# Optimization experiments

Measured on AMD Instinct MI355X. Metric: run time of the kernel, lower is better.

## Reference

```python
import jax, jax.numpy as jnp
import numpy as np

DT_SCALER = 1.0 / 24.0
ODE_STEPS = 4  # fixed-step RK4 stand-in for adaptive odeint(rtol=atol=1e-3)
B, T, D, H = 1024, 100, 32, 256
ODE_MID = 50  # hidden width of the ODE func MLP (hard-coded 50 in source)


def setup_inputs() -> dict:
    key = jax.random.key(0)
    ks = jax.random.split(key, 20)
    n = lambda k, s: jax.random.normal(k, s, dtype=jnp.float32)
    std = 0.1  # module inits weights N(0, 0.1), biases 0
    return {
        "dt": jax.random.uniform(ks[0], (B, T, 2), dtype=jnp.float32),
        "x": n(ks[1], (B, T, D)),
        # RNNCell params
        "W_ih": n(ks[2], (H, D)) * std,
        "b_ih": jnp.zeros((H,), jnp.float32),
        "W_hh": n(ks[3], (H, H)) * std,
        "b_hh": jnp.zeros((H,), jnp.float32),
        # ODE func: Linear(H,50) -> tanh -> Linear(50,H)
        "ode_w1": n(ks[4], (ODE_MID, H)) * std,
        "ode_b1": jnp.zeros((ODE_MID,), jnp.float32),
        "ode_w2": n(ks[5], (H, ODE_MID)) * std,
        "ode_b2": jnp.zeros((H,), jnp.float32),
        # mu head: l1 (H -> H//2), distribution_mu (H//2 -> 1)
        "l1_w": n(ks[6], (H // 2, H)) * std,
        "l1_b": jnp.zeros((H // 2,), jnp.float32),
        "mu_w": n(ks[7], (1, H // 2)) * std,
        "mu_b": jnp.zeros((1,), jnp.float32),
        # sigma head: Linear(H,H) -> tanh -> Linear(H,1) -> softplus
        "sig_w1": n(ks[8], (H, H)) * std,
        "sig_b1": jnp.zeros((H,), jnp.float32),
        "sig_w2": n(ks[9], (1, H)) * std,
        "sig_b2": jnp.zeros((1,), jnp.float32),
    }


def reference(dt, x, W_ih, b_ih, W_hh, b_hh, ode_w1, ode_b1, ode_w2, ode_b2,
              l1_w, l1_b, mu_w, mu_b, sig_w1, sig_b1, sig_w2, sig_b2):
    Bsz = x.shape[0]
    xs = jnp.swapaxes(x, 0, 1)                               # [T,B,D]
    dts = jnp.swapaxes(dt[:, :, 1] - dt[:, :, 0], 0, 1)[..., None]  # [T,B,1]
    h0 = jnp.zeros((Bsz, W_hh.shape[0]), x.dtype)
    hs = 1.0 / ODE_STEPS

    def ode_f(y, scale):
        # net(y) * (dt * DT_SCALER); RHS is time-independent
        return (jnp.tanh(y @ ode_w1.T + ode_b1) @ ode_w2.T + ode_b2) * scale

    def step(h, inp):
        x_i, dt_i = inp                                      # [B,D], [B,1]
        # h_t = h_t + RNNCell(x_i, h_t)
        h = h + jnp.tanh(x_i @ W_ih.T + b_ih + h @ W_hh.T + b_hh)
        scale = dt_i * DT_SCALER
        # integrate dh/dt = ode_f(h) from t=0 to t=1 (fixed-step RK4)
        def rk4(y, _):
            k1 = ode_f(y, scale)
            k2 = ode_f(y + 0.5 * hs * k1, scale)
            k3 = ode_f(y + 0.5 * hs * k2, scale)
            k4 = ode_f(y + hs * k3, scale)
            return y + (hs / 6.0) * (k1 + 2.0 * k2 + 2.0 * k3 + k4), None
        h, _ = jax.lax.scan(rk4, h, None, length=ODE_STEPS)
        # heads (eval mode: dropout is identity)
        mu = jax.nn.relu(h @ l1_w.T + l1_b) @ mu_w.T + mu_b              # [B,1]
        sig = jax.nn.softplus(jnp.tanh(h @ sig_w1.T + sig_b1) @ sig_w2.T + sig_b2)
        return h, (mu, sig)

    _, (mu_seq, sig_seq) = jax.lax.scan(step, h0, (xs, dts))
    mu_out = jnp.swapaxes(mu_seq, 0, 1)    # [B,T,1]
    sig_out = jnp.swapaxes(sig_seq, 0, 1)  # [B,T,1]
    return (mu_out, sig_out)
```

## Files before the change

### kernel.cpp

```cpp
#include <hip/hip_runtime.h>
#include <math.h>


#define NT 512

#define WF_WCAT 0
#define WF_L1   18432
#define WF_SG   26624

#define F4_YC   0
#define F4_MID  128
#define F4_HL   160
#define F4_X    416
#define F4_L1O  432
#define F4_SG   496
#define SM_L1B  2496
#define SM_SB1  2624
#define SM_MUW  2880
#define SM_SW2  3008
#define SM_SCL  3264
#define SM_TOTF 3272

__device__ __forceinline__ float fma4(float acc, float4 y, float4 w) {
  acc = fmaf(y.x, w.x, acc); acc = fmaf(y.y, w.y, acc);
  acc = fmaf(y.z, w.z, acc); acc = fmaf(y.w, w.w, acc);
  return acc;
}
__device__ __forceinline__ float4 add4(float4 a, float4 b) {
  return make_float4(a.x + b.x, a.y + b.y, a.z + b.z, a.w + b.w);
}
__device__ __forceinline__ float4 axpy4(float a, float4 xv, float4 yv) {
  return make_float4(fmaf(a, xv.x, yv.x), fmaf(a, xv.y, yv.y),
                     fmaf(a, xv.z, yv.z), fmaf(a, xv.w, yv.w));
}
__device__ __forceinline__ float4 muls4(float4 v, float s) {
  return make_float4(v.x * s, v.y * s, v.z * s, v.w * s);
}
__device__ __forceinline__ float tfast(float x) {
  float ax = fabsf(x);
  float e  = __expf(-2.f * ax);
  float t  = (1.f - e) * __builtin_amdgcn_rcpf(1.f + e);
  return copysignf(t, x);
}
__device__ __forceinline__ float4 tfast4(float4 v) {
  return make_float4(tfast(v.x), tfast(v.y), tfast(v.z), tfast(v.w));
}

template <int CTRL>
__device__ __forceinline__ float dpp_add(float v) {
  int s = __builtin_amdgcn_update_dpp(0, __float_as_int(v), CTRL, 0xF, 0xF, true);
  return v + __int_as_float(s);
}
__device__ __forceinline__ float red2(float v)  { return dpp_add<0xB1>(v); }
__device__ __forceinline__ float red4(float v)  { return dpp_add<0x4E>(dpp_add<0xB1>(v)); }
__device__ __forceinline__ float red8(float v)  {
  return dpp_add<0xB1>(dpp_add<0x4E>(dpp_add<0x141>(v)));
}
__device__ __forceinline__ float red16(float v) {
  return dpp_add<0xB1>(dpp_add<0x4E>(dpp_add<0x141>(dpp_add<0x140>(v))));
}

__global__ void prep_w(const float* __restrict__ Wih, const float* __restrict__ Whh,
                       const float* __restrict__ l1w, const float* __restrict__ sw1,
                       float* __restrict__ ws) {
  int i = blockIdx.x * 256 + threadIdx.x;
  if (i < 73728) {
    int fi = i >> 2, comp = i & 3;
    int j = fi >> 9, tw = fi & 511;
    int c = j / 9, gg = j - c * 9;
    int cq = tw >> 3, kc = tw & 7;
    int k = 36 * kc + 4 * gg + comp, col = 4 * cq + c;
    ws[i] = (k < 32) ? Wih[col * 32 + k] : Whh[col * 256 + (k - 32)];
  } else if (i < 73728 + 32768) {
    int t = i - 73728;
    int fi = t >> 2, comp = t & 3;
    int j = fi >> 7, tt = fi & 127;
    int c = j >> 4, jj = j & 15;
    int cq = tt >> 2, kc = tt & 3;
    int k = 4 * (4 * jj + kc) + comp, col = 4 * cq + c;
    ws[73728 + t] = l1w[col * 256 + k];
  } else if (i < 172032) {
    int t = i - 106496;
    int fi = t >> 2, comp = t & 3;
    int j = fi >> 7, tt = fi & 127;
    int c = j >> 5, jj = j & 31;
    int cq = tt >> 1, kc = tt & 1;
    int k = 4 * (2 * jj + kc) + comp, col = 4 * cq + c;
    ws[106496 + t] = sw1[col * 256 + k];
  }
}

__device__ __forceinline__ void rnn_phase(int tid, int pOld, const float4* __restrict__ wc4,
                                          float4* smf4, float4 bcR) {
  const int cq = tid >> 3, kc = tid & 7;
  float a0 = 0, a1 = 0, a2 = 0, a3 = 0, a4 = 0, a5 = 0, a6 = 0, a7 = 0;
#pragma unroll 1
  for (int gg = 0; gg < 9; ++gg) {
    int g = kc * 9 + gg;
    int i0 = (g < 8) ? (F4_X + g) : (F4_HL + pOld * 128 + (g - 8));
    int i1 = (g < 8) ? (F4_X + 8 + g) : (F4_HL + pOld * 128 + 64 + (g - 8));
    float4 y0 = smf4[i0];
    float4 y1 = smf4[i1];
    float4 w0 = wc4[(0 * 9 + gg) * 512 + tid];
    float4 w1 = wc4[(1 * 9 + gg) * 512 + tid];
    float4 w2 = wc4[(2 * 9 + gg) * 512 + tid];
    float4 w3 = wc4[(3 * 9 + gg) * 512 + tid];
    a0 = fma4(a0, y0, w0); a1 = fma4(a1, y0, w1);
    a2 = fma4(a2, y0, w2); a3 = fma4(a3, y0, w3);
    a4 = fma4(a4, y1, w0); a5 = fma4(a5, y1, w1);
    a6 = fma4(a6, y1, w2); a7 = fma4(a7, y1, w3);
  }
  a0 = red8(a0); a1 = red8(a1); a2 = red8(a2); a3 = red8(a3);
  a4 = red8(a4); a5 = red8(a5); a6 = red8(a6); a7 = red8(a7);
  if (kc == 0) {
    float4 h0 = smf4[F4_HL + pOld * 128 + cq];
    float4 h1 = smf4[F4_HL + pOld * 128 + 64 + cq];
    float4 n0 = add4(h0, tfast4(add4(make_float4(a0, a1, a2, a3), bcR)));
    float4 n1 = add4(h1, tfast4(add4(make_float4(a4, a5, a6, a7), bcR)));
    int pN = pOld ^ 1;
    smf4[F4_HL + pN * 128 + cq] = n0;
    smf4[F4_HL + pN * 128 + 64 + cq] = n1;
    smf4[F4_YC + cq] = n0;
    smf4[F4_YC + 64 + cq] = n1;
  }
}

__global__ __attribute__((amdgpu_flat_work_group_size(NT, NT)))
__attribute__((amdgpu_waves_per_eu(4)))
void odernn_main(const float* __restrict__ dt,
                 const float* __restrict__ x,
                 const float* __restrict__ bih,
                 const float* __restrict__ bhh,
                 const float* __restrict__ ow1,
                 const float* __restrict__ ob1g,
                 const float* __restrict__ ow2,
                 const float* __restrict__ ob2g,
                 const float* __restrict__ l1bg,
                 const float* __restrict__ muwg,
                 const float* __restrict__ mubg,
                 const float* __restrict__ sb1g,
                 const float* __restrict__ sw2g,
                 const float* __restrict__ sb2g,
                 const float* __restrict__ ws,
                 float* __restrict__ out) {
  __shared__ __align__(16) float sm[SM_TOTF];
  float4* smf4 = (float4*)sm;
  const int tid = threadIdx.x;
  const int b0 = blockIdx.x * 2;

  const float4* wc4  = (const float4*)ws + WF_WCAT;
  const float4* l1s4 = (const float4*)ws + WF_L1;
  const float4* sgs4 = (const float4*)ws + WF_SG;

  const int cqR = tid >> 3;
  float4 bcR = make_float4(bih[4 * cqR + 0] + bhh[4 * cqR + 0],
                           bih[4 * cqR + 1] + bhh[4 * cqR + 1],
                           bih[4 * cqR + 2] + bhh[4 * cqR + 2],
                           bih[4 * cqR + 3] + bhh[4 * cqR + 3]);

  if (tid < 128) { sm[SM_L1B + tid] = l1bg[tid]; sm[SM_MUW + tid] = muwg[tid]; }
  if (tid < 256) { sm[SM_SB1 + tid] = sb1g[tid]; sm[SM_SW2 + tid] = sw2g[tid]; }
  if (tid < 128) smf4[F4_HL + tid] = make_float4(0.f, 0.f, 0.f, 0.f);
  if (tid < 16) {
    int r = tid >> 3, g = tid & 7;
    smf4[F4_X + tid] = ((const float4*)x)[((size_t)(b0 + r) * 100) * 8 + g];
  } else if (tid < 18) {
    const float* dp = dt + ((size_t)(b0 + tid - 16) * 100) * 2;
    sm[SM_SCL + tid - 16] = (dp[1] - dp[0]) * (1.f / 24.f);
  }
  __syncthreads();

  if (tid < 256) {
    const int q1 = tid >> 4, kc1 = tid & 15;
    float4 w1r[16];
#pragma unroll
    for (int n = 0; n < 4; ++n) {
      int row = 4 * q1 + n;
#pragma unroll
      for (int j = 0; j < 4; ++j)
        w1r[n * 4 + j] = (row < 50)
            ? *(const float4*)&ow1[row * 256 + 64 * j + 4 * kc1]
            : make_float4(0.f, 0.f, 0.f, 0.f);
    }
    float4 ob1r = make_float4(4 * q1 + 0 < 50 ? ob1g[4 * q1 + 0] : 0.f,
                              4 * q1 + 1 < 50 ? ob1g[4 * q1 + 1] : 0.f,
                              4 * q1 + 2 < 50 ? ob1g[4 * q1 + 2] : 0.f,
                              4 * q1 + 3 < 50 ? ob1g[4 * q1 + 3] : 0.f);
    const int rH = tid >> 7, cqH = (tid >> 2) & 31, kcH = tid & 3;
    const int t7 = tid & 127;
    const float mubv = mubg[0];

    for (int t = 0; t < 100; ++t) {
      const int pOld = t & 1, pNew = pOld ^ 1;
      rnn_phase(tid, pOld, wc4, smf4, bcR);
      __syncthreads();
#pragma unroll 1
      for (int e = 0; e < 16; ++e) {
        float a0 = 0, a1 = 0, a2 = 0, a3 = 0, a4 = 0, a5 = 0, a6 = 0, a7 = 0;
#pragma unroll
        for (int j = 0; j < 4; ++j) {
          float4 y0 = smf4[F4_YC + 16 * j + kc1];
          float4 y1 = smf4[F4_YC + 64 + 16 * j + kc1];
          a0 = fma4(a0, y0, w1r[0 * 4 + j]); a1 = fma4(a1, y0, w1r[1 * 4 + j]);
          a2 = fma4(a2, y0, w1r[2 * 4 + j]); a3 = fma4(a3, y0, w1r[3 * 4 + j]);
          a4 = fma4(a4, y1, w1r[0 * 4 + j]); a5 = fma4(a5, y1, w1r[1 * 4 + j]);
          a6 = fma4(a6, y1, w1r[2 * 4 + j]); a7 = fma4(a7, y1, w1r[3 * 4 + j]);
        }
        a0 = red16(a0); a1 = red16(a1); a2 = red16(a2); a3 = red16(a3);
        a4 = red16(a4); a5 = red16(a5); a6 = red16(a6); a7 = red16(a7);
        if (kc1 == 0) {
          smf4[F4_MID + q1]      = tfast4(add4(make_float4(a0, a1, a2, a3), ob1r));
          smf4[F4_MID + 16 + q1] = tfast4(add4(make_float4(a4, a5, a6, a7), ob1r));
        }
        __syncthreads();
        __syncthreads();
      }
      float c0 = 0, c1 = 0, c2 = 0, c3 = 0;
#pragma unroll 2
      for (int jj = 0; jj < 16; ++jj) {
        float4 h = smf4[F4_HL + pNew * 128 + rH * 64 + 4 * jj + kcH];
        c0 = fma4(c0, h, l1s4[(0 * 16 + jj) * 128 + t7]);
        c1 = fma4(c1, h, l1s4[(1 * 16 + jj) * 128 + t7]);
        c2 = fma4(c2, h, l1s4[(2 * 16 + jj) * 128 + t7]);
        c3 = fma4(c3, h, l1s4[(3 * 16 + jj) * 128 + t7]);
      }
      c0 = red4(c0); c1 = red4(c1); c2 = red4(c2); c3 = red4(c3);
      if (kcH == 0) {
        float4 b = ((const float4*)(sm + SM_L1B))[cqH];
        float4 v = add4(make_float4(c0, c1, c2, c3), b);
        smf4[F4_L1O + rH * 32 + cqH] =
            make_float4(fmaxf(v.x, 0.f), fmaxf(v.y, 0.f), fmaxf(v.z, 0.f), fmaxf(v.w, 0.f));
      }
      if (t < 99) {
        if (tid < 16) {
          int r = tid >> 3, g = tid & 7;
          smf4[F4_X + tid] = ((const float4*)x)[((size_t)(b0 + r) * 100 + t + 1) * 8 + g];
        } else if (tid < 18) {
          const float* dp = dt + ((size_t)(b0 + tid - 16) * 100 + t + 1) * 2;
          sm[SM_SCL + tid - 16] = (dp[1] - dp[0]) * (1.f / 24.f);
        }
      }
      __syncthreads();
      int wv = tid >> 6, ln = tid & 63;
      if (wv < 2) {
        float pm = 0.f;
        if (ln < 32) {
          float4 l = smf4[F4_L1O + wv * 32 + ln];
          float4 w = ((const float4*)(sm + SM_MUW))[ln];
          pm = l.x * w.x + l.y * w.y + l.z * w.z + l.w * w.w;
        }
#pragma unroll
        for (int off = 32; off > 0; off >>= 1) pm += __shfl_down(pm, off);
        if (ln == 0) out[(size_t)(b0 + wv) * 100 + t] = pm + mubv;
      }
    }
  } else {
    const int tid2 = tid - 256;
    const int cqB = tid2 >> 2, kc2 = tid2 & 3;
    float4 w2r[16];
#pragma unroll
    for (int c = 0; c < 4; ++c) {
      int col = 4 * cqB + c;
#pragma unroll
      for (int j = 0; j < 4; ++j) {
        float w0v[4];
#pragma unroll
        for (int cc = 0; cc < 4; ++cc) {
          int k = 16 * j + 4 * kc2 + cc;
          w0v[cc] = (k < 50) ? ow2[col * 50 + k] : 0.f;
        }
        w2r[c * 4 + j] = make_float4(w0v[0], w0v[1], w0v[2], w0v[3]);
      }
    }
    float4 ob2r = make_float4(ob2g[4 * cqB + 0], ob2g[4 * cqB + 1],
                              ob2g[4 * cqB + 2], ob2g[4 * cqB + 3]);
    const int rH = tid2 >> 7, cqH = (tid2 >> 1) & 63, kcH = tid2 & 1;
    const int t7 = tid2 & 127;
    const float sb2v = sb2g[0];

    for (int t = 0; t < 100; ++t) {
      const int pOld = t & 1, pNew = pOld ^ 1;
      rnn_phase(tid, pOld, wc4, smf4, bcR);
      __syncthreads();
      float s0 = sm[SM_SCL + 0], s1 = sm[SM_SCL + 1];
      float4 h0 = smf4[F4_YC + cqB];
      float4 h1 = smf4[F4_YC + 64 + cqB];
      float4 ac0 = make_float4(0, 0, 0, 0), ac1 = ac0;
#pragma unroll 1
      for (int os = 0; os < 4; ++os) {
#pragma unroll
        for (int s = 0; s < 4; ++s) {
          __syncthreads();
          float b0 = 0, b1 = 0, b2 = 0, b3 = 0, b4 = 0, b5 = 0, b6 = 0, b7 = 0;
#pragma unroll
          for (int j = 0; j < 4; ++j) {
            float4 m0 = smf4[F4_MID + 4 * j + kc2];
            float4 m1 = smf4[F4_MID + 16 + 4 * j + kc2];
            b0 = fma4(b0, m0, w2r[0 * 4 + j]); b1 = fma4(b1, m0, w2r[1 * 4 + j]);
            b2 = fma4(b2, m0, w2r[2 * 4 + j]); b3 = fma4(b3, m0, w2r[3 * 4 + j]);
            b4 = fma4(b4, m1, w2r[0 * 4 + j]); b5 = fma4(b5, m1, w2r[1 * 4 + j]);
            b6 = fma4(b6, m1, w2r[2 * 4 + j]); b7 = fma4(b7, m1, w2r[3 * 4 + j]);
          }
          b0 = red4(b0); b1 = red4(b1); b2 = red4(b2); b3 = red4(b3);
          b4 = red4(b4); b5 = red4(b5); b6 = red4(b6); b7 = red4(b7);
          float4 k0 = muls4(add4(make_float4(b0, b1, b2, b3), ob2r), s0);
          float4 k1 = muls4(add4(make_float4(b4, b5, b6, b7), ob2r), s1);
          float4 y0w, y1w;
          if (s == 0) {
            ac0 = k0; ac1 = k1;
            y0w = axpy4(0.125f, k0, h0); y1w = axpy4(0.125f, k1, h1);
          } else if (s == 1) {
            ac0 = axpy4(2.f, k0, ac0); ac1 = axpy4(2.f, k1, ac1);
            y0w = axpy4(0.125f, k0, h0); y1w = axpy4(0.125f, k1, h1);
          } else if (s == 2) {
            ac0 = axpy4(2.f, k0, ac0); ac1 = axpy4(2.f, k1, ac1);
            y0w = axpy4(0.25f, k0, h0); y1w = axpy4(0.25f, k1, h1);
          } else {
            h0 = axpy4(0.25f / 6.f, add4(ac0, k0), h0);
            h1 = axpy4(0.25f / 6.f, add4(ac1, k1), h1);
            y0w = h0; y1w = h1;
          }
          if (kc2 == 0) {
            smf4[F4_YC + cqB] = y0w;
            smf4[F4_YC + 64 + cqB] = y1w;
            if (os == 3 && s == 3) {
              smf4[F4_HL + pNew * 128 + cqB] = h0;
              smf4[F4_HL + pNew * 128 + 64 + cqB] = h1;
            }
          }
          __syncthreads();
        }
      }
      float d0 = 0, d1 = 0, d2 = 0, d3 = 0;
#pragma unroll 2
      for (int jj = 0; jj < 32; ++jj) {
        float4 h = smf4[F4_HL + pNew * 128 + rH * 64 + 2 * jj + kcH];
        d0 = fma4(d0, h, sgs4[(0 * 32 + jj) * 128 + t7]);
        d1 = fma4(d1, h, sgs4[(1 * 32 + jj) * 128 + t7]);
        d2 = fma4(d2, h, sgs4[(2 * 32 + jj) * 128 + t7]);
        d3 = fma4(d3, h, sgs4[(3 * 32 + jj) * 128 + t7]);
      }
      d0 = red2(d0); d1 = red2(d1); d2 = red2(d2); d3 = red2(d3);
      if (kcH == 0) {
        float4 sb = ((const float4*)(sm + SM_SB1))[cqH];
        smf4[F4_SG + rH * 64 + cqH] = tfast4(add4(make_float4(d0, d1, d2, d3), sb));
      }
      __syncthreads();
      int wv = tid >> 6, ln = tid & 63;
      if (wv < 6) {
        int r = wv - 4;
        float4 sv = smf4[F4_SG + r * 64 + ln];
        float4 w = ((const float4*)(sm + SM_SW2))[ln];
        float ps = sv.x * w.x + sv.y * w.y + sv.z * w.z + sv.w * w.w;
#pragma unroll
        for (int off = 32; off > 0; off >>= 1) ps += __shfl_down(ps, off);
        if (ln == 0) {
          float z = ps + sb2v;
          float sp = fmaxf(z, 0.f) + log1pf(expf(-fabsf(z)));
          out[(size_t)102400 + (size_t)(b0 + r) * 100 + t] = sp;
        }
      }
    }
  }
}

extern "C" void kernel_launch(void* const* d_in, const int* in_sizes, int n_in,
                              void* d_out, int out_size, void* d_ws, size_t ws_size,
                              hipStream_t stream) {
  const float* dt  = (const float*)d_in[0];
  const float* x   = (const float*)d_in[1];
  const float* Wih = (const float*)d_in[2];
  const float* bih = (const float*)d_in[3];
  const float* Whh = (const float*)d_in[4];
  const float* bhh = (const float*)d_in[5];
  const float* ow1 = (const float*)d_in[6];
  const float* ob1 = (const float*)d_in[7];
  const float* ow2 = (const float*)d_in[8];
  const float* ob2 = (const float*)d_in[9];
  const float* l1w = (const float*)d_in[10];
  const float* l1b = (const float*)d_in[11];
  const float* muw = (const float*)d_in[12];
  const float* mub = (const float*)d_in[13];
  const float* sw1 = (const float*)d_in[14];
  const float* sb1 = (const float*)d_in[15];
  const float* sw2 = (const float*)d_in[16];
  const float* sb2 = (const float*)d_in[17];
  float* ws  = (float*)d_ws;
  float* out = (float*)d_out;

  prep_w<<<672, 256, 0, stream>>>(Wih, Whh, l1w, sw1, ws);
  odernn_main<<<512, NT, 0, stream>>>(dt, x, bih, bhh, ow1, ob1, ow2, ob2,
                                      l1b, muw, mub, sb1, sw2, sb2, ws, out);
}
```

Before: 3.806 ms.

## Process four batch rows per block with ping-pong ODE layer pipelining

New measurement: 4.371 ms. 1.15x slower.

```diff
diff --git a/kernel.cpp b/kernel.cpp
--- a/kernel.cpp
+++ b/kernel.cpp
@@ -8,18 +8,20 @@
 #define WF_L1   18432
 #define WF_SG   26624
 
-#define F4_YC   0
-#define F4_MID  128
-#define F4_HL   160
-#define F4_X    416
-#define F4_L1O  432
-#define F4_SG   496
-#define SM_L1B  2496
-#define SM_SB1  2624
-#define SM_MUW  2880
-#define SM_SW2  3008
-#define SM_SCL  3264
-#define SM_TOTF 3272
+#define F4_YCP  0
+#define F4_YCQ  128
+#define F4_MIDP 256
+#define F4_MIDQ 288
+#define F4_HL   320
+#define F4_X    832
+#define F4_L1O  896
+#define F4_SG   1024
+#define SM_L1B  5120
+#define SM_SB1  5248
+#define SM_MUW  5504
+#define SM_SW2  5632
+#define SM_SCL  5888
+#define SM_TOTF 5896
 
 __device__ __forceinline__ float fma4(float acc, float4 y, float4 w) {
   acc = fmaf(y.x, w.x, acc); acc = fmaf(y.y, w.y, acc);
@@ -45,7 +47,6 @@
 __device__ __forceinline__ float4 tfast4(float4 v) {
   return make_float4(tfast(v.x), tfast(v.y), tfast(v.z), tfast(v.w));
 }
-
 template <int CTRL>
 __device__ __forceinline__ float dpp_add(float v) {
   int s = __builtin_amdgcn_update_dpp(0, __float_as_int(v), CTRL, 0xF, 0xF, true);
@@ -71,62 +72,70 @@
     int cq = tw >> 3, kc = tw & 7;
     int k = 36 * kc + 4 * gg + comp, col = 4 * cq + c;
     ws[i] = (k < 32) ? Wih[col * 32 + k] : Whh[col * 256 + (k - 32)];
-  } else if (i < 73728 + 32768) {
+  } else if (i < 106496) {
     int t = i - 73728;
     int fi = t >> 2, comp = t & 3;
-    int j = fi >> 7, tt = fi & 127;
-    int c = j >> 4, jj = j & 15;
-    int cq = tt >> 2, kc = tt & 3;
-    int k = 4 * (4 * jj + kc) + comp, col = 4 * cq + c;
+    int low = fi & 63, rest = fi >> 6;
+    int c = rest >> 5, jj = rest & 31;
+    int cqH = low >> 1, kcH = low & 1;
+    int col = 4 * cqH + c, k = 4 * (32 * kcH + jj) + comp;
     ws[73728 + t] = l1w[col * 256 + k];
-  } else if (i < 172032) {
+  } else {
     int t = i - 106496;
     int fi = t >> 2, comp = t & 3;
-    int j = fi >> 7, tt = fi & 127;
-    int c = j >> 5, jj = j & 31;
-    int cq = tt >> 1, kc = tt & 1;
-    int k = 4 * (2 * jj + kc) + comp, col = 4 * cq + c;
+    int cqB = fi & 63, rest = fi >> 6;
+    int c = rest >> 6, kq = rest & 63;
+    int col = 4 * cqB + c, k = 4 * kq + comp;
     ws[106496 + t] = sw1[col * 256 + k];
   }
 }
 
-__device__ __forceinline__ void rnn_phase(int tid, int pOld, const float4* __restrict__ wc4,
-                                          float4* smf4, float4 bcR) {
+__device__ __forceinline__ void rnn_phase4(int tid, int pOld,
+                                           const float4* __restrict__ wc4,
+                                           float4* smf4, float4 bcR) {
   const int cq = tid >> 3, kc = tid & 7;
-  float a0 = 0, a1 = 0, a2 = 0, a3 = 0, a4 = 0, a5 = 0, a6 = 0, a7 = 0;
+  float a00=0,a01=0,a02=0,a03=0, a10=0,a11=0,a12=0,a13=0;
+  float a20=0,a21=0,a22=0,a23=0, a30=0,a31=0,a32=0,a33=0;
 #pragma unroll 1
   for (int gg = 0; gg < 9; ++gg) {
     int g = kc * 9 + gg;
-    int i0 = (g < 8) ? (F4_X + g) : (F4_HL + pOld * 128 + (g - 8));
-    int i1 = (g < 8) ? (F4_X + 8 + g) : (F4_HL + pOld * 128 + 64 + (g - 8));
-    float4 y0 = smf4[i0];
-    float4 y1 = smf4[i1];
     float4 w0 = wc4[(0 * 9 + gg) * 512 + tid];
     float4 w1 = wc4[(1 * 9 + gg) * 512 + tid];
     float4 w2 = wc4[(2 * 9 + gg) * 512 + tid];
     float4 w3 = wc4[(3 * 9 + gg) * 512 + tid];
-    a0 = fma4(a0, y0, w0); a1 = fma4(a1, y0, w1);
-    a2 = fma4(a2, y0, w2); a3 = fma4(a3, y0, w3);
-    a4 = fma4(a4, y1, w0); a5 = fma4(a5, y1, w1);
-    a6 = fma4(a6, y1, w2); a7 = fma4(a7, y1, w3);
+    float4 y0, y1, y2, y3;
+    if (g < 8) {
+      const int xb = F4_X + pOld * 32;
+      y0 = smf4[xb + g]; y1 = smf4[xb + 8 + g];
+      y2 = smf4[xb + 16 + g]; y3 = smf4[xb + 24 + g];
+    } else {
+      const int hb = F4_HL + pOld * 256 + (g - 8);
+      y0 = smf4[hb]; y1 = smf4[hb + 64];
+      y2 = smf4[hb + 128]; y3 = smf4[hb + 192];
+    }
+    a00=fma4(a00,y0,w0); a01=fma4(a01,y0,w1); a02=fma4(a02,y0,w2); a03=fma4(a03,y0,w3);
+    a10=fma4(a10,y1,w0); a11=fma4(a11,y1,w1); a12=fma4(a12,y1,w2); a13=fma4(a13,y1,w3);
+    a20=fma4(a20,y2,w0); a21=fma4(a21,y2,w1); a22=fma4(a22,y2,w2); a23=fma4(a23,y2,w3);
+    a30=fma4(a30,y3,w0); a31=fma4(a31,y3,w1); a32=fma4(a32,y3,w2); a33=fma4(a33,y3,w3);
   }
-  a0 = red8(a0); a1 = red8(a1); a2 = red8(a2); a3 = red8(a3);
-  a4 = red8(a4); a5 = red8(a5); a6 = red8(a6); a7 = red8(a7);
+  a00=red8(a00); a01=red8(a01); a02=red8(a02); a03=red8(a03);
+  a10=red8(a10); a11=red8(a11); a12=red8(a12); a13=red8(a13);
+  a20=red8(a20); a21=red8(a21); a22=red8(a22); a23=red8(a23);
+  a30=red8(a30); a31=red8(a31); a32=red8(a32); a33=red8(a33);
   if (kc == 0) {
-    float4 h0 = smf4[F4_HL + pOld * 128 + cq];
-    float4 h1 = smf4[F4_HL + pOld * 128 + 64 + cq];
-    float4 n0 = add4(h0, tfast4(add4(make_float4(a0, a1, a2, a3), bcR)));
-    float4 n1 = add4(h1, tfast4(add4(make_float4(a4, a5, a6, a7), bcR)));
-    int pN = pOld ^ 1;
-    smf4[F4_HL + pN * 128 + cq] = n0;
-    smf4[F4_HL + pN * 128 + 64 + cq] = n1;
-    smf4[F4_YC + cq] = n0;
-    smf4[F4_YC + 64 + cq] = n1;
+    const int hb = F4_HL + pOld * 256;
+    float4 h0 = smf4[hb + cq],       h1 = smf4[hb + 64 + cq];
+    float4 h2 = smf4[hb + 128 + cq], h3 = smf4[hb + 192 + cq];
+    float4 n0 = add4(h0, tfast4(add4(make_float4(a00,a01,a02,a03), bcR)));
+    float4 n1 = add4(h1, tfast4(add4(make_float4(a10,a11,a12,a13), bcR)));
+    float4 n2 = add4(h2, tfast4(add4(make_float4(a20,a21,a22,a23), bcR)));
+    float4 n3 = add4(h3, tfast4(add4(make_float4(a30,a31,a32,a33), bcR)));
+    smf4[F4_YCP + cq] = n0; smf4[F4_YCP + 64 + cq] = n1;
+    smf4[F4_YCQ + cq] = n2; smf4[F4_YCQ + 64 + cq] = n3;
   }
 }
 
 __global__ __attribute__((amdgpu_flat_work_group_size(NT, NT)))
-__attribute__((amdgpu_waves_per_eu(4)))
 void odernn_main(const float* __restrict__ dt,
                  const float* __restrict__ x,
                  const float* __restrict__ bih,
@@ -146,11 +155,12 @@
   __shared__ __align__(16) float sm[SM_TOTF];
   float4* smf4 = (float4*)sm;
   const int tid = threadIdx.x;
-  const int b0 = blockIdx.x * 2;
+  const int b0 = blockIdx.x * 4;
 
   const float4* wc4  = (const float4*)ws + WF_WCAT;
   const float4* l1s4 = (const float4*)ws + WF_L1;
   const float4* sgs4 = (const float4*)ws + WF_SG;
+  const float4* xg4  = (const float4*)x;
 
   const int cqR = tid >> 3;
   float4 bcR = make_float4(bih[4 * cqR + 0] + bhh[4 * cqR + 0],
@@ -160,13 +170,14 @@
 
   if (tid < 128) { sm[SM_L1B + tid] = l1bg[tid]; sm[SM_MUW + tid] = muwg[tid]; }
   if (tid < 256) { sm[SM_SB1 + tid] = sb1g[tid]; sm[SM_SW2 + tid] = sw2g[tid]; }
-  if (tid < 128) smf4[F4_HL + tid] = make_float4(0.f, 0.f, 0.f, 0.f);
-  if (tid < 16) {
+  if (tid < 256) smf4[F4_HL + tid] = make_float4(0.f, 0.f, 0.f, 0.f);
+  if (tid < 32) {
     int r = tid >> 3, g = tid & 7;
-    smf4[F4_X + tid] = ((const float4*)x)[((size_t)(b0 + r) * 100) * 8 + g];
-  } else if (tid < 18) {
-    const float* dp = dt + ((size_t)(b0 + tid - 16) * 100) * 2;
-    sm[SM_SCL + tid - 16] = (dp[1] - dp[0]) * (1.f / 24.f);
+    smf4[F4_X + tid] = xg4[((size_t)(b0 + r) * 100) * 8 + g];
+  } else if (tid < 36) {
+    int r = tid - 32;
+    const float* dp = dt + ((size_t)(b0 + r) * 100) * 2;
+    sm[SM_SCL + r] = (dp[1] - dp[0]) * (1.f / 24.f);
   }
   __syncthreads();
 
@@ -186,63 +197,59 @@
                               4 * q1 + 1 < 50 ? ob1g[4 * q1 + 1] : 0.f,
                               4 * q1 + 2 < 50 ? ob1g[4 * q1 + 2] : 0.f,
                               4 * q1 + 3 < 50 ? ob1g[4 * q1 + 3] : 0.f);
-    const int rH = tid >> 7, cqH = (tid >> 2) & 31, kcH = tid & 3;
-    const int t7 = tid & 127;
+    const int wv = tid >> 6, ln = tid & 63;
+    const int rH = tid >> 6, low = tid & 63, cqH = low >> 1, kcH = low & 1;
     const float mubv = mubg[0];
 
     for (int t = 0; t < 100; ++t) {
       const int pOld = t & 1, pNew = pOld ^ 1;
-      rnn_phase(tid, pOld, wc4, smf4, bcR);
+      rnn_phase4(tid, pOld, wc4, smf4, bcR);
       __syncthreads();
-#pragma unroll 1
-      for (int e = 0; e < 16; ++e) {
-        float a0 = 0, a1 = 0, a2 = 0, a3 = 0, a4 = 0, a5 = 0, a6 = 0, a7 = 0;
-#pragma unroll
-        for (int j = 0; j < 4; ++j) {
-          float4 y0 = smf4[F4_YC + 16 * j + kc1];
-          float4 y1 = smf4[F4_YC + 64 + 16 * j + kc1];
-          a0 = fma4(a0, y0, w1r[0 * 4 + j]); a1 = fma4(a1, y0, w1r[1 * 4 + j]);
-          a2 = fma4(a2, y0, w1r[2 * 4 + j]); a3 = fma4(a3, y0, w1r[3 * 4 + j]);
-          a4 = fma4(a4, y1, w1r[0 * 4 + j]); a5 = fma4(a5, y1, w1r[1 * 4 + j]);
-          a6 = fma4(a6, y1, w1r[2 * 4 + j]); a7 = fma4(a7, y1, w1r[3 * 4 + j]);
-        }
-        a0 = red16(a0); a1 = red16(a1); a2 = red16(a2); a3 = red16(a3);
-        a4 = red16(a4); a5 = red16(a5); a6 = red16(a6); a7 = red16(a7);
-        if (kc1 == 0) {
-          smf4[F4_MID + q1]      = tfast4(add4(make_float4(a0, a1, a2, a3), ob1r));
-          smf4[F4_MID + 16 + q1] = tfast4(add4(make_float4(a4, a5, a6, a7), ob1r));
+      for (int ph = 0; ph < 33; ++ph) {
+        if (ph < 32) {
+          const int ycB = (ph & 1) ? F4_YCQ : F4_YCP;
+          const int mdB = (ph & 1) ? F4_MIDQ : F4_MIDP;
+          float a0 = 0, a1 = 0, a2 = 0, a3 = 0, a4 = 0, a5 = 0, a6 = 0, a7 = 0;
+#pragma unroll
+          for (int j = 0; j < 4; ++j) {
+            float4 y0 = smf4[ycB + 16 * j + kc1];
+            float4 y1 = smf4[ycB + 64 + 16 * j + kc1];
+            a0 = fma4(a0, y0, w1r[0 * 4 + j]); a1 = fma4(a1, y0, w1r[1 * 4 + j]);
+            a2 = fma4(a2, y0, w1r[2 * 4 + j]); a3 = fma4(a3, y0, w1r[3 * 4 + j]);
+            a4 = fma4(a4, y1, w1r[0 * 4 + j]); a5 = fma4(a5, y1, w1r[1 * 4 + j]);
+            a6 = fma4(a6, y1, w1r[2 * 4 + j]); a7 = fma4(a7, y1, w1r[3 * 4 + j]);
+          }
+          a0 = red16(a0); a1 = red16(a1); a2 = red16(a2); a3 = red16(a3);
+          a4 = red16(a4); a5 = red16(a5); a6 = red16(a6); a7 = red16(a7);
+          if (kc1 == 0) {
+            smf4[mdB + q1]      = tfast4(add4(make_float4(a0, a1, a2, a3), ob1r));
+            smf4[mdB + 16 + q1] = tfast4(add4(make_float4(a4, a5, a6, a7), ob1r));
+          }
         }
         __syncthreads();
-        __syncthreads();
-      }
-      float c0 = 0, c1 = 0, c2 = 0, c3 = 0;
+      }
+      {
+        float c0 = 0, c1 = 0, c2 = 0, c3 = 0;
+        const float4* hrow = smf4 + F4_HL + pNew * 256 + rH * 64 + kcH * 32;
 #pragma unroll 2
-      for (int jj = 0; jj < 16; ++jj) {
-        float4 h = smf4[F4_HL + pNew * 128 + rH * 64 + 4 * jj + kcH];
-        c0 = fma4(c0, h, l1s4[(0 * 16 + jj) * 128 + t7]);
-        c1 = fma4(c1, h, l1s4[(1 * 16 + jj) * 128 + t7]);
-        c2 = fma4(c2, h, l1s4[(2 * 16 + jj) * 128 + t7]);
-        c3 = fma4(c3, h, l1s4[(3 * 16 + jj) * 128 + t7]);
-      }
-      c0 = red4(c0); c1 = red4(c1); c2 = red4(c2); c3 = red4(c3);
-      if (kcH == 0) {
-        float4 b = ((const float4*)(sm + SM_L1B))[cqH];
-        float4 v = add4(make_float4(c0, c1, c2, c3), b);
-        smf4[F4_L1O + rH * 32 + cqH] =
-            make_float4(fmaxf(v.x, 0.f), fmaxf(v.y, 0.f), fmaxf(v.z, 0.f), fmaxf(v.w, 0.f));
-      }
-      if (t < 99) {
-        if (tid < 16) {
-          int r = tid >> 3, g = tid & 7;
-          smf4[F4_X + tid] = ((const float4*)x)[((size_t)(b0 + r) * 100 + t + 1) * 8 + g];
-        } else if (tid < 18) {
-          const float* dp = dt + ((size_t)(b0 + tid - 16) * 100 + t + 1) * 2;
-          sm[SM_SCL + tid - 16] = (dp[1] - dp[0]) * (1.f / 24.f);
+        for (int jj = 0; jj < 32; ++jj) {
+          float4 h = hrow[jj];
+          c0 = fma4(c0, h, l1s4[(0 * 32 + jj) * 64 + low]);
+          c1 = fma4(c1, h, l1s4[(1 * 32 + jj) * 64 + low]);
+          c2 = fma4(c2, h, l1s4[(2 * 32 + jj) * 64 + low]);
+          c3 = fma4(c3, h, l1s4[(3 * 32 + jj) * 64 + low]);
+        }
+        c0 = red2(c0); c1 = red2(c1); c2 = red2(c2); c3 = red2(c3);
+        if (kcH == 0) {
+          float4 b = ((const float4*)(sm + SM_L1B))[cqH];
+          float4 v = add4(make_float4(c0, c1, c2, c3), b);
+          smf4[F4_L1O + rH * 32 + cqH] =
+              make_float4(fmaxf(v.x, 0.f), fmaxf(v.y, 0.f),
+                          fmaxf(v.z, 0.f), fmaxf(v.w, 0.f));
         }
       }
       __syncthreads();
-      int wv = tid >> 6, ln = tid & 63;
-      if (wv < 2) {
+      {
         float pm = 0.f;
         if (ln < 32) {
           float4 l = smf4[F4_L1O + wv * 32 + ln];
@@ -263,92 +270,111 @@
       int col = 4 * cqB + c;
 #pragma unroll
       for (int j = 0; j < 4; ++j) {
-        float w0v[4];
+        float wt[4];
 #pragma unroll
         for (int cc = 0; cc < 4; ++cc) {
           int k = 16 * j + 4 * kc2 + cc;
-          w0v[cc] = (k < 50) ? ow2[col * 50 + k] : 0.f;
-        }
-        w2r[c * 4 + j] = make_float4(w0v[0], w0v[1], w0v[2], w0v[3]);
+          wt[cc] = (k < 50) ? ow2[col * 50 + k] : 0.f;
+        }
+        w2r[c * 4 + j] = make_float4(wt[0], wt[1], wt[2], wt[3]);
       }
     }
     float4 ob2r = make_float4(ob2g[4 * cqB + 0], ob2g[4 * cqB + 1],
                               ob2g[4 * cqB + 2], ob2g[4 * cqB + 3]);
-    const int rH = tid2 >> 7, cqH = (tid2 >> 1) & 63, kcH = tid2 & 1;
-    const int t7 = tid2 & 127;
+    const int wv = tid >> 6, ln = tid & 63;
+    const int rH2 = tid2 >> 6, cqS = tid2 & 63;
     const float sb2v = sb2g[0];
 
     for (int t = 0; t < 100; ++t) {
       const int pOld = t & 1, pNew = pOld ^ 1;
-      rnn_phase(tid, pOld, wc4, smf4, bcR);
+      rnn_phase4(tid, pOld, wc4, smf4, bcR);
       __syncthreads();
-      float s0 = sm[SM_SCL + 0], s1 = sm[SM_SCL + 1];
-      float4 h0 = smf4[F4_YC + cqB];
-      float4 h1 = smf4[F4_YC + 64 + cqB];
-      float4 ac0 = make_float4(0, 0, 0, 0), ac1 = ac0;
-#pragma unroll 1
-      for (int os = 0; os < 4; ++os) {
-#pragma unroll
-        for (int s = 0; s < 4; ++s) {
-          __syncthreads();
-          float b0 = 0, b1 = 0, b2 = 0, b3 = 0, b4 = 0, b5 = 0, b6 = 0, b7 = 0;
-#pragma unroll
-          for (int j = 0; j < 4; ++j) {
-            float4 m0 = smf4[F4_MID + 4 * j + kc2];
-            float4 m1 = smf4[F4_MID + 16 + 4 * j + kc2];
-            b0 = fma4(b0, m0, w2r[0 * 4 + j]); b1 = fma4(b1, m0, w2r[1 * 4 + j]);
-            b2 = fma4(b2, m0, w2r[2 * 4 + j]); b3 = fma4(b3, m0, w2r[3 * 4 + j]);
-            b4 = fma4(b4, m1, w2r[0 * 4 + j]); b5 = fma4(b5, m1, w2r[1 * 4 + j]);
-            b6 = fma4(b6, m1, w2r[2 * 4 + j]); b7 = fma4(b7, m1, w2r[3 * 4 + j]);
+      float sc0 = sm[SM_SCL + pOld * 4 + 0], sc1 = sm[SM_SCL + pOld * 4 + 1];
+      float sc2 = sm[SM_SCL + pOld * 4 + 2], sc3 = sm[SM_SCL + pOld * 4 + 3];
+      float4 hP0 = smf4[F4_YCP + cqB], hP1 = smf4[F4_YCP + 64 + cqB];
+      float4 hQ0 = smf4[F4_YCQ + cqB], hQ1 = smf4[F4_YCQ + 64 + cqB];
+      float4 acP0 = make_float4(0, 0, 0, 0), acP1 = acP0, acQ0 = acP0, acQ1 = acP0;
+      if (t < 99) {
+        if (tid2 < 32) {
+          int r = tid2 >> 3, g = tid2 & 7;
+          smf4[F4_X + pNew * 32 + tid2] = xg4[((size_t)(b0 + r) * 100 + t + 1) * 8 + g];
+        } else if (tid2 < 36) {
+          int r = tid2 - 32;
+          const float* dp = dt + ((size_t)(b0 + r) * 100 + t + 1) * 2;
+          sm[SM_SCL + pNew * 4 + r] = (dp[1] - dp[0]) * (1.f / 24.f);
+        }
+      }
+      __syncthreads();
+
+      auto l2eval = [&](float4& h0, float4& h1, float4& ac0, float4& ac1,
+                        float s0, float s1, int mdB, int ycB, int hlB,
+                        int s, bool last) {
+        float b0 = 0, b1 = 0, b2 = 0, b3 = 0, b4 = 0, b5 = 0, b6 = 0, b7 = 0;
+#pragma unroll
+        for (int j = 0; j < 4; ++j) {
+          float4 m0 = smf4[mdB + 4 * j + kc2];
+          float4 m1 = smf4[mdB + 16 + 4 * j + kc2];
+          b0 = fma4(b0, m0, w2r[0 * 4 + j]); b1 = fma4(b1, m0, w2r[1 * 4 + j]);
+          b2 = fma4(b2, m0, w2r[2 * 4 + j]); b3 = fma4(b3, m0, w2r[3 * 4 + j]);
+          b4 = fma4(b4, m1, w2r[0 * 4 + j]); b5 = fma4(b5, m1, w2r[1 * 4 + j]);
+          b6 = fma4(b6, m1, w2r[2 * 4 + j]); b7 = fma4(b7, m1, w2r[3 * 4 + j]);
+        }
+        b0 = red4(b0); b1 = red4(b1); b2 = red4(b2); b3 = red4(b3);
+        b4 = red4(b4); b5 = red4(b5); b6 = red4(b6); b7 = red4(b7);
+        float4 k0 = muls4(add4(make_float4(b0, b1, b2, b3), ob2r), s0);
+        float4 k1 = muls4(add4(make_float4(b4, b5, b6, b7), ob2r), s1);
+        float4 y0w, y1w;
+        if (s == 0) {
+          ac0 = k0; ac1 = k1;
+          y0w = axpy4(0.125f, k0, h0); y1w = axpy4(0.125f, k1, h1);
+        } else if (s == 1) {
+          ac0 = axpy4(2.f, k0, ac0); ac1 = axpy4(2.f, k1, ac1);
+          y0w = axpy4(0.125f, k0, h0); y1w = axpy4(0.125f, k1, h1);
+        } else if (s == 2) {
+          ac0 = axpy4(2.f, k0, ac0); ac1 = axpy4(2.f, k1, ac1);
+          y0w = axpy4(0.25f, k0, h0); y1w = axpy4(0.25f, k1, h1);
+        } else {
+          h0 = axpy4(0.25f / 6.f, add4(ac0, k0), h0);
+          h1 = axpy4(0.25f / 6.f, add4(ac1, k1), h1);
+          y0w = h0; y1w = h1;
+        }
+        if (kc2 == 0) {
+          smf4[ycB + cqB] = y0w;
+          smf4[ycB + 64 + cqB] = y1w;
+          if (last) {
+            smf4[hlB + cqB] = h0;
+            smf4[hlB + 64 + cqB] = h1;
           }
-          b0 = red4(b0); b1 = red4(b1); b2 = red4(b2); b3 = red4(b3);
-          b4 = red4(b4); b5 = red4(b5); b6 = red4(b6); b7 = red4(b7);
-          float4 k0 = muls4(add4(make_float4(b0, b1, b2, b3), ob2r), s0);
-          float4 k1 = muls4(add4(make_float4(b4, b5, b6, b7), ob2r), s1);
-          float4 y0w, y1w;
-          if (s == 0) {
-            ac0 = k0; ac1 = k1;
-            y0w = axpy4(0.125f, k0, h0); y1w = axpy4(0.125f, k1, h1);
-          } else if (s == 1) {
-            ac0 = axpy4(2.f, k0, ac0); ac1 = axpy4(2.f, k1, ac1);
-            y0w = axpy4(0.125f, k0, h0); y1w = axpy4(0.125f, k1, h1);
-          } else if (s == 2) {
-            ac0 = axpy4(2.f, k0, ac0); ac1 = axpy4(2.f, k1, ac1);
-            y0w = axpy4(0.25f, k0, h0); y1w = axpy4(0.25f, k1, h1);
-          } else {
-            h0 = axpy4(0.25f / 6.f, add4(ac0, k0), h0);
-            h1 = axpy4(0.25f / 6.f, add4(ac1, k1), h1);
-            y0w = h0; y1w = h1;
-          }
-          if (kc2 == 0) {
-            smf4[F4_YC + cqB] = y0w;
-            smf4[F4_YC + 64 + cqB] = y1w;
-            if (os == 3 && s == 3) {
-              smf4[F4_HL + pNew * 128 + cqB] = h0;
-              smf4[F4_HL + pNew * 128 + 64 + cqB] = h1;
-            }
-          }
-          __syncthreads();
-        }
-      }
-      float d0 = 0, d1 = 0, d2 = 0, d3 = 0;
+        }
+      };
+
+      for (int ph = 1; ph <= 32; ++ph) {
+        const int e = (ph - 1) >> 1, s = e & 3;
+        if (ph & 1)
+          l2eval(hP0, hP1, acP0, acP1, sc0, sc1, F4_MIDP, F4_YCP,
+                 F4_HL + pNew * 256, s, e == 15);
+        else
+          l2eval(hQ0, hQ1, acQ0, acQ1, sc2, sc3, F4_MIDQ, F4_YCQ,
+                 F4_HL + pNew * 256 + 128, s, e == 15);
+        __syncthreads();
+      }
+      {
+        float d0 = 0, d1 = 0, d2 = 0, d3 = 0;
+        const float4* hrow = smf4 + F4_HL + pNew * 256 + rH2 * 64;
 #pragma unroll 2
-      for (int jj = 0; jj < 32; ++jj) {
-        float4 h = smf4[F4_HL + pNew * 128 + rH * 64 + 2 * jj + kcH];
-        d0 = fma4(d0, h, sgs4[(0 * 32 + jj) * 128 + t7]);
-        d1 = fma4(d1, h, sgs4[(1 * 32 + jj) * 128 + t7]);
-        d2 = fma4(d2, h, sgs4[(2 * 32 + jj) * 128 + t7]);
-        d3 = fma4(d3, h, sgs4[(3 * 32 + jj) * 128 + t7]);
-      }
-      d0 = red2(d0); d1 = red2(d1); d2 = red2(d2); d3 = red2(d3);
-      if (kcH == 0) {
-        float4 sb = ((const float4*)(sm + SM_SB1))[cqH];
-        smf4[F4_SG + rH * 64 + cqH] = tfast4(add4(make_float4(d0, d1, d2, d3), sb));
+        for (int kq = 0; kq < 64; ++kq) {
+          float4 h = hrow[kq];
+          d0 = fma4(d0, h, sgs4[(0 * 64 + kq) * 64 + cqS]);
+          d1 = fma4(d1, h, sgs4[(1 * 64 + kq) * 64 + cqS]);
+          d2 = fma4(d2, h, sgs4[(2 * 64 + kq) * 64 + cqS]);
+          d3 = fma4(d3, h, sgs4[(3 * 64 + kq) * 64 + cqS]);
+        }
+        float4 sb = ((const float4*)(sm + SM_SB1))[cqS];
+        smf4[F4_SG + rH2 * 64 + cqS] = tfast4(add4(make_float4(d0, d1, d2, d3), sb));
       }
       __syncthreads();
-      int wv = tid >> 6, ln = tid & 63;
-      if (wv < 6) {
-        int r = wv - 4;
+      {
+        const int r = wv - 4;
         float4 sv = smf4[F4_SG + r * 64 + ln];
         float4 w = ((const float4*)(sm + SM_SW2))[ln];
         float ps = sv.x * w.x + sv.y * w.y + sv.z * w.z + sv.w * w.w;
@@ -389,6 +415,6 @@
   float* out = (float*)d_out;
 
   prep_w<<<672, 256, 0, stream>>>(Wih, Whh, l1w, sw1, ws);
-  odernn_main<<<512, NT, 0, stream>>>(dt, x, bih, bhh, ow1, ob1, ow2, ob2,
+  odernn_main<<<256, NT, 0, stream>>>(dt, x, bih, bhh, ow1, ob1, ow2, ob2,
                                       l1b, muw, mub, sb1, sw2, sb2, ws, out);
 }
```
